# Optimization experiments

Hardware: AMD Instinct MI355X
Metric: run time of the kernel (lower is better)

Reference implementation:

```python
import jax, jax.numpy as jnp
import numpy as np

N_NODES = 50000
N_EDGES = 800000
IN_C, HID_C, OUT_C = 128, 128, 64


def setup_inputs() -> dict:
    key = jax.random.key(0)
    ks = jax.random.split(key, 12)
    glorot = lambda k, shape: jax.random.normal(k, shape, dtype=jnp.float32) * (2.0 / (shape[0] + shape[-1])) ** 0.5
    return {
        "x": jax.random.normal(ks[0], (N_NODES, IN_C), dtype=jnp.float32),
        "edge_index": jax.random.randint(ks[1], (2, N_EDGES), 0, N_NODES, dtype=jnp.int64),
        "W_s1": glorot(ks[2], (IN_C, HID_C)), "b_s1": jnp.zeros((HID_C,), jnp.float32),
        "W_s2": glorot(ks[3], (HID_C, HID_C)), "b_s2": jnp.zeros((HID_C,), jnp.float32),
        "W_m1": glorot(ks[4], (IN_C, HID_C)), "b_m1": jnp.zeros((HID_C,), jnp.float32),
        "W_m21": glorot(ks[5], (IN_C, HID_C)), "b_m21": jnp.zeros((HID_C,), jnp.float32),
        "W_m22": glorot(ks[6], (HID_C, HID_C)), "b_m22": jnp.zeros((HID_C,), jnp.float32),
        "W_att": glorot(ks[7], (HID_C, 1)), "b_att": jnp.zeros((1,), jnp.float32),
        "W_fc": glorot(ks[8], (2 * HID_C, OUT_C)), "b_fc": jnp.zeros((OUT_C,), jnp.float32),
    }


def _gcn_conv(x, W, b, src, dst, n_nodes):
    """PyG GCNConv: add self-loops, symmetric deg^-1/2 norm, linear, scatter-add, bias."""
    xw = x @ W  # [N, H]
    loop = jnp.arange(n_nodes, dtype=src.dtype)
    s = jnp.concatenate([src, loop])
    d = jnp.concatenate([dst, loop])
    ones = jnp.ones(s.shape[0], dtype=x.dtype)
    deg = jax.ops.segment_sum(ones, d, num_segments=n_nodes)  # in-degree incl. self loop
    dinv = jnp.where(deg > 0, jax.lax.rsqrt(deg), 0.0)
    norm = dinv[s] * dinv[d]  # [E+N]
    msg = xw[s] * norm[:, None]
    return jax.ops.segment_sum(msg, d, num_segments=n_nodes) + b


def reference(x, edge_index, W_s1, b_s1, W_s2, b_s2, W_m1, b_m1, W_m21, b_m21,
              W_m22, b_m22, W_att, b_att, W_fc, b_fc):
    n = x.shape[0]
    src, dst = edge_index[0], edge_index[1]
    # structural branch: two GCN layers
    h_struct = jax.nn.relu(_gcn_conv(x, W_s1, b_s1, src, dst, n))
    h_struct = jax.nn.relu(_gcn_conv(h_struct, W_s2, b_s2, src, dst, n))
    # meta branches
    h1 = jax.nn.relu(_gcn_conv(x, W_m1, b_m1, src, dst, n))
    h2 = jax.nn.relu(_gcn_conv(x, W_m21, b_m21, src, dst, n))
    h2 = jax.nn.relu(_gcn_conv(h2, W_m22, b_m22, src, dst, n))
    # attention-weighted fusion over the 2 branches
    H = jnp.stack([h1, h2], axis=1)  # [N, 2, H]
    attn_scores = H @ W_att + b_att  # [N, 2, 1]
    attn_weights = jax.nn.softmax(attn_scores, axis=1)
    h_meta = jnp.sum(attn_weights * H, axis=1)  # [N, H]
    h_comb = jnp.concatenate([h_struct, h_meta], axis=1)  # [N, 2H]
    return h_comb @ W_fc + b_fc  # [N, OUT_C]
```

## Files before the change

### kernel.cpp

```cpp
#include <hip/hip_runtime.h>
#include <hip/hip_bf16.h>

#define N_NODES 50000
#define N_EDGES 800000
#define IN_C 128
#define HID_C 128
#define OUT_C 64

#define SCAN_BS 256
#define SCAN_NB ((N_NODES + SCAN_BS - 1) / SCAN_BS)

typedef __attribute__((ext_vector_type(8))) short bf16x8;
typedef __attribute__((ext_vector_type(4))) float f32x4;

__device__ __forceinline__ ushort f2bf(float f) {
    unsigned u = __float_as_uint(f);
    return (ushort)((u + 0x7fffu + ((u >> 16) & 1u)) >> 16);
}
__device__ __forceinline__ float bf2f(ushort u) {
    return __uint_as_float(((unsigned)u) << 16);
}

__global__ void degree_kernel(const int* __restrict__ dst, int E, int* __restrict__ hist) {
    int e = blockIdx.x * blockDim.x + threadIdx.x;
    if (e < E) atomicAdd(&hist[dst[e]], 1);
}

__global__ void dinv_kernel(const int* __restrict__ hist, float* __restrict__ dinv, int n) {
    int i = blockIdx.x * blockDim.x + threadIdx.x;
    if (i < n) dinv[i] = rsqrtf((float)(hist[i] + 1));
}

__global__ __launch_bounds__(SCAN_BS)
void scan1_kernel(const int* __restrict__ hist, int* __restrict__ bsum, int n) {
    __shared__ int s[SCAN_BS];
    int t = threadIdx.x;
    int i = blockIdx.x * SCAN_BS + t;
    int v = (i < n) ? hist[i] : 0;
    s[t] = v;
    __syncthreads();
#pragma unroll
    for (int off = SCAN_BS / 2; off > 0; off >>= 1) {
        if (t < off) s[t] += s[t + off];
        __syncthreads();
    }
    if (t == 0) bsum[blockIdx.x] = s[0];
}

__global__ __launch_bounds__(SCAN_BS)
void scan2_kernel(int* __restrict__ bsum, int* __restrict__ bpre, int nb,
                  int* __restrict__ row_ptr_last, int n) {
    __shared__ int s[SCAN_BS];
    int t = threadIdx.x;
    int v = (t < nb) ? bsum[t] : 0;
    s[t] = v;
    __syncthreads();
#pragma unroll
    for (int off = 1; off < SCAN_BS; off <<= 1) {
        int tmp = (t >= off) ? s[t - off] : 0;
        __syncthreads();
        s[t] += tmp;
        __syncthreads();
    }
    if (t < nb) bpre[t] = s[t] - v;
    if (t == SCAN_BS - 1) row_ptr_last[n] = s[t];
}

__global__ __launch_bounds__(SCAN_BS)
void scan3_kernel(const int* __restrict__ hist, const int* __restrict__ bpre,
                  int* __restrict__ row_ptr, int* __restrict__ cursor, int n) {
    __shared__ int s[SCAN_BS];
    int t = threadIdx.x;
    int i = blockIdx.x * SCAN_BS + t;
    int v = (i < n) ? hist[i] : 0;
    s[t] = v;
    __syncthreads();
#pragma unroll
    for (int off = 1; off < SCAN_BS; off <<= 1) {
        int tmp = (t >= off) ? s[t - off] : 0;
        __syncthreads();
        s[t] += tmp;
        __syncthreads();
    }
    if (i < n) {
        int ex = s[t] - v + bpre[blockIdx.x];
        row_ptr[i] = ex;
        cursor[i]  = ex;
    }
}

__global__ void fill_kernel(const int* __restrict__ src, const int* __restrict__ dst, int E,
                            int* __restrict__ cursor, int2* __restrict__ edge_data,
                            const float* __restrict__ dinv) {
    int e = blockIdx.x * blockDim.x + threadIdx.x;
    if (e < E) {
        int d = dst[e];
        int s = src[e];
        int pos = atomicAdd(&cursor[d], 1);
        edge_data[pos] = make_int2(s, __float_as_int(dinv[s]));
    }
}

__global__ void cvt_bf16_kernel(const float* __restrict__ in, uint2* __restrict__ out, int n4) {
    int i = blockIdx.x * blockDim.x + threadIdx.x;
    if (i >= n4) return;
    float4 v = *(const float4*)&in[(size_t)i * 4];
    uint2 o;
    o.x = (uint)f2bf(v.x) | ((uint)f2bf(v.y) << 16);
    o.y = (uint)f2bf(v.z) | ((uint)f2bf(v.w) << 16);
    out[i] = o;
}

__global__ void pack_wcat_kernel(const float* __restrict__ Ws1, const float* __restrict__ Wm21,
                                 const float* __restrict__ Wm1,
                                 const float* __restrict__ bs1, const float* __restrict__ bm21,
                                 const float* __restrict__ bm1,
                                 ushort* __restrict__ Wt, float* __restrict__ bcat) {
    int idx = blockIdx.x * blockDim.x + threadIdx.x;
    if (idx < 384 * 128) {
        int c = idx >> 7, k = idx & 127;
        float v = (c < 128) ? Ws1[k * 128 + c]
                : (c < 256) ? Wm21[k * 128 + (c - 128)]
                            : Wm1[k * 128 + (c - 256)];
        Wt[idx] = f2bf(v);
    }
    if (idx < 384) {
        bcat[idx] = (idx < 128) ? bs1[idx] : (idx < 256) ? bm21[idx - 128] : bm1[idx - 256];
    }
}

__global__ void tpack_kernel(const float* __restrict__ W, ushort* __restrict__ Wt, int K, int C) {
    int idx = blockIdx.x * blockDim.x + threadIdx.x;
    if (idx >= K * C) return;
    int c = idx / K, k = idx % K;
    Wt[idx] = f2bf(W[(size_t)k * C + c]);
}

template<int C>
__global__ __launch_bounds__(256)
void agg_bf16(const ushort* __restrict__ X, int ldx,
              ushort* __restrict__ Y, int ldy,
              const int* __restrict__ row_ptr,
              const int2* __restrict__ edge_data,
              const float* __restrict__ dinv, int n) {
    constexpr int CG = C / 8;
    constexpr int SLOTS = 64 / CG;
    const int wid = blockIdx.x * (blockDim.x >> 6) + (threadIdx.x >> 6);
    if (wid >= n) return;
    const int lane = threadIdx.x & 63;
    const int cg = lane & (CG - 1);
    const int slot = lane / CG;

    const float di = dinv[wid];
    float acc[8] = {0.f, 0.f, 0.f, 0.f, 0.f, 0.f, 0.f, 0.f};

    auto fma_row = [&](uint4 v, float w) {
        acc[0] = fmaf(w, __uint_as_float(v.x << 16), acc[0]);
        acc[1] = fmaf(w, __uint_as_float(v.x & 0xffff0000u), acc[1]);
        acc[2] = fmaf(w, __uint_as_float(v.y << 16), acc[2]);
        acc[3] = fmaf(w, __uint_as_float(v.y & 0xffff0000u), acc[3]);
        acc[4] = fmaf(w, __uint_as_float(v.z << 16), acc[4]);
        acc[5] = fmaf(w, __uint_as_float(v.z & 0xffff0000u), acc[5]);
        acc[6] = fmaf(w, __uint_as_float(v.w << 16), acc[6]);
        acc[7] = fmaf(w, __uint_as_float(v.w & 0xffff0000u), acc[7]);
    };

    if (slot == 0) {
        uint4 v = *(const uint4*)&X[(size_t)wid * ldx + cg * 8];
        fma_row(v, di * di);
    }
    const int e0 = row_ptr[wid], e1 = row_ptr[wid + 1];
    int e = e0 + slot;
    for (; e + 3 * SLOTS < e1; e += 4 * SLOTS) {
        const int2 d0 = edge_data[e];
        const int2 d1 = edge_data[e + SLOTS];
        const int2 d2 = edge_data[e + 2 * SLOTS];
        const int2 d3 = edge_data[e + 3 * SLOTS];
        const uint4 v0 = *(const uint4*)&X[(size_t)d0.x * ldx + cg * 8];
        const uint4 v1 = *(const uint4*)&X[(size_t)d1.x * ldx + cg * 8];
        const uint4 v2 = *(const uint4*)&X[(size_t)d2.x * ldx + cg * 8];
        const uint4 v3 = *(const uint4*)&X[(size_t)d3.x * ldx + cg * 8];
        fma_row(v0, di * __int_as_float(d0.y));
        fma_row(v1, di * __int_as_float(d1.y));
        fma_row(v2, di * __int_as_float(d2.y));
        fma_row(v3, di * __int_as_float(d3.y));
    }
    for (; e < e1; e += SLOTS) {
        const int2 d0 = edge_data[e];
        const uint4 v0 = *(const uint4*)&X[(size_t)d0.x * ldx + cg * 8];
        fma_row(v0, di * __int_as_float(d0.y));
    }
#pragma unroll
    for (int j = 0; j < 8; ++j) {
        if (SLOTS == 4) acc[j] += __shfl_xor(acc[j], 16);
        if (SLOTS >= 2) acc[j] += __shfl_xor(acc[j], 32);
    }
    if (slot == 0) {
        uint4 o;
        o.x = (uint)f2bf(acc[0]) | ((uint)f2bf(acc[1]) << 16);
        o.y = (uint)f2bf(acc[2]) | ((uint)f2bf(acc[3]) << 16);
        o.z = (uint)f2bf(acc[4]) | ((uint)f2bf(acc[5]) << 16);
        o.w = (uint)f2bf(acc[6]) | ((uint)f2bf(acc[7]) << 16);
        *(uint4*)&Y[(size_t)wid * ldy + cg * 8] = o;
    }
}

__global__ __launch_bounds__(256)
void mfma_gemm_kernel(const ushort* __restrict__ A, int lda,
                      const ushort* __restrict__ Wt,
                      const float* __restrict__ bias,
                      void* __restrict__ Yv, int ldy,
                      int M, int relu, int obf16) {
    __shared__ char Asmem[128 * 272];
    const int tid = threadIdx.x;
    const int lane = tid & 63;
    const int w = tid >> 6;
    const int rb = blockIdx.x * 128;
    const int cb = blockIdx.y * 128;

    {
        const int rowbase = tid >> 4;
        const int inrow = (tid & 15) * 8;
#pragma unroll
        for (int it = 0; it < 8; ++it) {
            int row = it * 16 + rowbase;
            uint4 v = make_uint4(0u, 0u, 0u, 0u);
            int r = rb + row;
            if (r < M) v = *(const uint4*)&A[(size_t)r * lda + inrow];
            *(uint4*)&Asmem[row * 272 + (tid & 15) * 16] = v;
        }
    }
    __syncthreads();

    f32x4 acc[2][8];
#pragma unroll
    for (int i = 0; i < 2; ++i)
#pragma unroll
        for (int j = 0; j < 8; ++j) acc[i][j] = (f32x4){0.f, 0.f, 0.f, 0.f};

    const int arow0 = w * 32 + (lane & 15);
    const int kq = (lane >> 4) * 8;
    const int ccol = lane & 15;
#pragma unroll
    for (int ks = 0; ks < 4; ++ks) {
        const int k0 = ks * 32;
        const bf16x8 a0 = *(const bf16x8*)&Asmem[arow0 * 272 + (k0 + kq) * 2];
        const bf16x8 a1 = *(const bf16x8*)&Asmem[(arow0 + 16) * 272 + (k0 + kq) * 2];
#pragma unroll
        for (int ct = 0; ct < 8; ++ct) {
            const bf16x8 b = *(const bf16x8*)&Wt[(size_t)(cb + ct * 16 + ccol) * 128 + k0 + kq];
            acc[0][ct] = __builtin_amdgcn_mfma_f32_16x16x32_bf16(a0, b, acc[0][ct], 0, 0, 0);
            acc[1][ct] = __builtin_amdgcn_mfma_f32_16x16x32_bf16(a1, b, acc[1][ct], 0, 0, 0);
        }
    }

    const int rowq = (lane >> 4) * 4;
#pragma unroll
    for (int rt = 0; rt < 2; ++rt) {
#pragma unroll
        for (int ct = 0; ct < 8; ++ct) {
            const int col = cb + ct * 16 + ccol;
            const float bcol = bias[col];
#pragma unroll
            for (int r = 0; r < 4; ++r) {
                const int row = rb + w * 32 + rt * 16 + rowq + r;
                if (row >= M) continue;
                float v = acc[rt][ct][r] + bcol;
                if (relu) v = fmaxf(v, 0.f);
                if (obf16) ((ushort*)Yv)[(size_t)row * ldy + col] = f2bf(v);
                else       ((float*)Yv)[(size_t)row * ldy + col] = v;
            }
        }
    }
}

__global__ __launch_bounds__(256)
void mfma_fc_kernel(const ushort* __restrict__ A,
                    const ushort* __restrict__ Wt,
                    const float* __restrict__ bias,
                    float* __restrict__ Y, int M) {
    __shared__ char Asmem[64 * 528];
    const int tid = threadIdx.x;
    const int lane = tid & 63;
    const int w = tid >> 6;
    const int rb = blockIdx.x * 64;

    {
        const int rowbase = tid >> 5;
        const int seg = (tid & 31);
#pragma unroll
        for (int it = 0; it < 8; ++it) {
            int row = it * 8 + rowbase;
            uint4 v = make_uint4(0u, 0u, 0u, 0u);
            int r = rb + row;
            if (r < M) v = *(const uint4*)&A[(size_t)r * 256 + seg * 8];
            *(uint4*)&Asmem[row * 528 + seg * 16] = v;
        }
    }
    __syncthreads();

    f32x4 acc[4];
#pragma unroll
    for (int j = 0; j < 4; ++j) acc[j] = (f32x4){0.f, 0.f, 0.f, 0.f};

    const int arow = w * 16 + (lane & 15);
    const int kq = (lane >> 4) * 8;
    const int ccol = lane & 15;
#pragma unroll
    for (int ks = 0; ks < 8; ++ks) {
        const int k0 = ks * 32;
        const bf16x8 a = *(const bf16x8*)&Asmem[arow * 528 + (k0 + kq) * 2];
#pragma unroll
        for (int ct = 0; ct < 4; ++ct) {
            const bf16x8 b = *(const bf16x8*)&Wt[(size_t)(ct * 16 + ccol) * 256 + k0 + kq];
            acc[ct] = __builtin_amdgcn_mfma_f32_16x16x32_bf16(a, b, acc[ct], 0, 0, 0);
        }
    }

    const int rowq = (lane >> 4) * 4;
#pragma unroll
    for (int ct = 0; ct < 4; ++ct) {
        const int col = ct * 16 + ccol;
        const float bcol = bias[col];
#pragma unroll
        for (int r = 0; r < 4; ++r) {
            const int row = rb + w * 16 + rowq + r;
            if (row < M) Y[(size_t)row * 64 + col] = acc[ct][r] + bcol;
        }
    }
}

__global__ __launch_bounds__(64)
void attn_kernel(const ushort* __restrict__ h1bf, const ushort* __restrict__ h2bf,
                 const float* __restrict__ Watt, const float* __restrict__ batt,
                 ushort* __restrict__ outb, int ldout) {
    int i = blockIdx.x;
    int l = threadIdx.x;
    const ushort* h1p = &h1bf[(size_t)i * 384 + 256];
    const ushort* h2p = &h2bf[(size_t)i * 128];
    float w0 = Watt[l], w1w = Watt[l + 64];
    float h1a = bf2f(h1p[l]), h1b = bf2f(h1p[l + 64]);
    float h2a = bf2f(h2p[l]), h2b = bf2f(h2p[l + 64]);
    float a = h1a * w0 + h1b * w1w;
    float b = h2a * w0 + h2b * w1w;
#pragma unroll
    for (int off = 32; off > 0; off >>= 1) {
        a += __shfl_xor(a, off);
        b += __shfl_xor(b, off);
    }
    float ba = batt[0];
    a += ba; b += ba;
    float m  = fmaxf(a, b);
    float ea = __expf(a - m), eb = __expf(b - m);
    float inv = 1.f / (ea + eb);
    float wa = ea * inv, wb = eb * inv;
    outb[(size_t)i * ldout + l]      = f2bf(wa * h1a + wb * h2a);
    outb[(size_t)i * ldout + l + 64] = f2bf(wa * h1b + wb * h2b);
}

extern "C" void kernel_launch(void* const* d_in, const int* in_sizes, int n_in,
                              void* d_out, int out_size, void* d_ws, size_t ws_size,
                              hipStream_t stream) {
    const int N = N_NODES, E = N_EDGES;
    const float* x     = (const float*)d_in[0];
    const int*   ei    = (const int*)d_in[1];
    const int*   esrc  = ei;
    const int*   edst  = ei + E;
    const float* W_s1  = (const float*)d_in[2];
    const float* b_s1  = (const float*)d_in[3];
    const float* W_s2  = (const float*)d_in[4];
    const float* b_s2  = (const float*)d_in[5];
    const float* W_m1  = (const float*)d_in[6];
    const float* b_m1  = (const float*)d_in[7];
    const float* W_m21 = (const float*)d_in[8];
    const float* b_m21 = (const float*)d_in[9];
    const float* W_m22 = (const float*)d_in[10];
    const float* b_m22 = (const float*)d_in[11];
    const float* W_att = (const float*)d_in[12];
    const float* b_att = (const float*)d_in[13];
    const float* W_fc  = (const float*)d_in[14];
    const float* b_fc  = (const float*)d_in[15];
    float* out = (float*)d_out;

    char* base = (char*)d_ws;
    size_t off = 0;
    auto take = [&](size_t nbytes) -> void* {
        void* p = base + off;
        off += (nbytes + 255) & ~(size_t)255;
        return p;
    };
    int*    hist      = (int*)take((size_t)N * 4);
    int*    cursor    = (int*)take((size_t)N * 4);
    int*    row_ptr   = (int*)take((size_t)(N + 1) * 4);
    int*    bsum      = (int*)take((size_t)SCAN_NB * 4);
    int*    bpre      = (int*)take((size_t)SCAN_NB * 4);
    int2*   edge_data = (int2*)take((size_t)E * 8);
    float*  dinv      = (float*)take((size_t)N * 4);
    ushort* xb        = (ushort*)take((size_t)N * 128 * 2);
    ushort* agg_x     = (ushort*)take((size_t)N * 128 * 2);
    ushort* cat1      = (ushort*)take((size_t)N * 384 * 2);
    ushort* bufB      = (ushort*)take((size_t)N * 256 * 2);
    ushort* comb      = (ushort*)take((size_t)N * 256 * 2);
    ushort* h2buf     = (ushort*)take((size_t)N * 128 * 2);
    ushort* Wcat_t    = (ushort*)take((size_t)384 * 128 * 2);
    ushort* Ws2_t     = (ushort*)take((size_t)128 * 128 * 2);
    ushort* Wm22_t    = (ushort*)take((size_t)128 * 128 * 2);
    ushort* Wfc_t     = (ushort*)take((size_t)64 * 256 * 2);
    float*  bcat      = (float*)take((size_t)384 * 4);

    hipMemsetAsync(hist, 0, (size_t)N * 4, stream);
    degree_kernel<<<(E + 255) / 256, 256, 0, stream>>>(edst, E, hist);
    dinv_kernel<<<(N + 255) / 256, 256, 0, stream>>>(hist, dinv, N);
    scan1_kernel<<<SCAN_NB, SCAN_BS, 0, stream>>>(hist, bsum, N);
    scan2_kernel<<<1, SCAN_BS, 0, stream>>>(bsum, bpre, SCAN_NB, row_ptr, N);
    scan3_kernel<<<SCAN_NB, SCAN_BS, 0, stream>>>(hist, bpre, row_ptr, cursor, N);
    fill_kernel<<<(E + 255) / 256, 256, 0, stream>>>(esrc, edst, E, cursor, edge_data, dinv);

    cvt_bf16_kernel<<<(N * 128 / 4 + 255) / 256, 256, 0, stream>>>(x, (uint2*)xb, N * 128 / 4);
    pack_wcat_kernel<<<(384 * 128 + 255) / 256, 256, 0, stream>>>(W_s1, W_m21, W_m1,
                                                                  b_s1, b_m21, b_m1, Wcat_t, bcat);
    tpack_kernel<<<(128 * 128 + 255) / 256, 256, 0, stream>>>(W_s2, Ws2_t, 128, 128);
    tpack_kernel<<<(128 * 128 + 255) / 256, 256, 0, stream>>>(W_m22, Wm22_t, 128, 128);
    tpack_kernel<<<(256 * 64 + 255) / 256, 256, 0, stream>>>(W_fc, Wfc_t, 256, 64);

    agg_bf16<128><<<(N + 3) / 4, 256, 0, stream>>>(xb, 128, agg_x, 128, row_ptr, edge_data, dinv, N);

    dim3 gm384((N + 127) / 128, 3);
    dim3 gm128((N + 127) / 128, 1);
    mfma_gemm_kernel<<<gm384, 256, 0, stream>>>(agg_x, 128, Wcat_t, bcat, cat1, 384, N, 1, 1);

    agg_bf16<256><<<(N + 3) / 4, 256, 0, stream>>>(cat1, 384, bufB, 256, row_ptr, edge_data, dinv, N);

    mfma_gemm_kernel<<<gm128, 256, 0, stream>>>(bufB, 256, Ws2_t, b_s2, comb, 256, N, 1, 1);
    mfma_gemm_kernel<<<gm128, 256, 0, stream>>>(bufB + 128, 256, Wm22_t, b_m22, h2buf, 128, N, 1, 1);

    attn_kernel<<<N, 64, 0, stream>>>(cat1, h2buf, W_att, b_att, comb + 128, 256);

    mfma_fc_kernel<<<(N + 63) / 64, 256, 0, stream>>>(comb, Wfc_t, b_fc, out, N);
}
```

Measured before the change: 414.0 us.

## Fuse preprocessing kernels, collapse scan passes, and fuse second-layer GEMMs with attention

Merges x conversion, degree histogram and all weight packing into one multi-role prep kernel, and folds the dinv computation into scan1. The single-block scan2 is removed: each scan3 block now sums the preceding block totals itself. The two second-layer GEMMs and the attention fusion kernel become one gemm2 kernel whose second branch computes the attention softmax in its epilogue, so the h2 intermediate buffer is gone. This cuts launch count and one round-trip of h2 through memory, at the cost of redundant prefix summation in scan3 and an extra read of h1 in the GEMM epilogue.

```diff
diff --git a/kernel.cpp b/kernel.cpp
--- a/kernel.cpp
+++ b/kernel.cpp
@@ -10,6 +10,12 @@
 #define SCAN_BS 256
 #define SCAN_NB ((N_NODES + SCAN_BS - 1) / SCAN_BS)
 
+#define PREP_CVT_NB   6250
+#define PREP_DEG_NB   3125
+#define PREP_WCAT_NB  192
+#define PREP_TP_NB    64
+#define PREP_NB (PREP_CVT_NB + PREP_DEG_NB + PREP_WCAT_NB + 3 * PREP_TP_NB)
+
 typedef __attribute__((ext_vector_type(8))) short bf16x8;
 typedef __attribute__((ext_vector_type(4))) float f32x4;
 
@@ -21,22 +27,64 @@
     return __uint_as_float(((unsigned)u) << 16);
 }
 
-__global__ void degree_kernel(const int* __restrict__ dst, int E, int* __restrict__ hist) {
-    int e = blockIdx.x * blockDim.x + threadIdx.x;
-    if (e < E) atomicAdd(&hist[dst[e]], 1);
-}
-
-__global__ void dinv_kernel(const int* __restrict__ hist, float* __restrict__ dinv, int n) {
-    int i = blockIdx.x * blockDim.x + threadIdx.x;
-    if (i < n) dinv[i] = rsqrtf((float)(hist[i] + 1));
+__global__ __launch_bounds__(256)
+void prep_kernel(const float* __restrict__ x, uint2* __restrict__ xb4,
+                 const int* __restrict__ edst, int* __restrict__ hist,
+                 const float* __restrict__ Ws1, const float* __restrict__ Wm21,
+                 const float* __restrict__ Wm1,
+                 const float* __restrict__ bs1, const float* __restrict__ bm21,
+                 const float* __restrict__ bm1,
+                 ushort* __restrict__ Wcat_t, float* __restrict__ bcat,
+                 const float* __restrict__ Ws2, ushort* __restrict__ Ws2t,
+                 const float* __restrict__ Wm22, ushort* __restrict__ Wm22t,
+                 const float* __restrict__ Wfc, ushort* __restrict__ Wfct,
+                 int* __restrict__ row_ptr) {
+    const int bid = blockIdx.x;
+    const int t = threadIdx.x;
+    if (bid < PREP_CVT_NB) {
+        int i = bid * 256 + t;
+        float4 v = *(const float4*)&x[(size_t)i * 4];
+        uint2 o;
+        o.x = (uint)f2bf(v.x) | ((uint)f2bf(v.y) << 16);
+        o.y = (uint)f2bf(v.z) | ((uint)f2bf(v.w) << 16);
+        xb4[i] = o;
+    } else if (bid < PREP_CVT_NB + PREP_DEG_NB) {
+        int e = (bid - PREP_CVT_NB) * 256 + t;
+        atomicAdd(&hist[edst[e]], 1);
+    } else if (bid < PREP_CVT_NB + PREP_DEG_NB + PREP_WCAT_NB) {
+        int idx = (bid - PREP_CVT_NB - PREP_DEG_NB) * 256 + t;
+        int c = idx >> 7, k = idx & 127;
+        float v = (c < 128) ? Ws1[k * 128 + c]
+                : (c < 256) ? Wm21[k * 128 + (c - 128)]
+                            : Wm1[k * 128 + (c - 256)];
+        Wcat_t[idx] = f2bf(v);
+        if (idx < 384) {
+            bcat[idx] = (idx < 128) ? bs1[idx] : (idx < 256) ? bm21[idx - 128] : bm1[idx - 256];
+        }
+        if (idx == 0) row_ptr[N_NODES] = N_EDGES;
+    } else if (bid < PREP_CVT_NB + PREP_DEG_NB + PREP_WCAT_NB + PREP_TP_NB) {
+        int idx = (bid - PREP_CVT_NB - PREP_DEG_NB - PREP_WCAT_NB) * 256 + t;
+        int c = idx >> 7, k = idx & 127;
+        Ws2t[idx] = f2bf(Ws2[(size_t)k * 128 + c]);
+    } else if (bid < PREP_CVT_NB + PREP_DEG_NB + PREP_WCAT_NB + 2 * PREP_TP_NB) {
+        int idx = (bid - PREP_CVT_NB - PREP_DEG_NB - PREP_WCAT_NB - PREP_TP_NB) * 256 + t;
+        int c = idx >> 7, k = idx & 127;
+        Wm22t[idx] = f2bf(Wm22[(size_t)k * 128 + c]);
+    } else {
+        int idx = (bid - PREP_CVT_NB - PREP_DEG_NB - PREP_WCAT_NB - 2 * PREP_TP_NB) * 256 + t;
+        int c = idx >> 8, k = idx & 255;
+        Wfct[idx] = f2bf(Wfc[(size_t)k * 64 + c]);
+    }
 }
 
 __global__ __launch_bounds__(SCAN_BS)
-void scan1_kernel(const int* __restrict__ hist, int* __restrict__ bsum, int n) {
+void scan1_kernel(const int* __restrict__ hist, int* __restrict__ bsum,
+                  float* __restrict__ dinv, int n) {
     __shared__ int s[SCAN_BS];
     int t = threadIdx.x;
     int i = blockIdx.x * SCAN_BS + t;
     int v = (i < n) ? hist[i] : 0;
+    if (i < n) dinv[i] = rsqrtf((float)(v + 1));
     s[t] = v;
     __syncthreads();
 #pragma unroll
@@ -48,11 +96,27 @@
 }
 
 __global__ __launch_bounds__(SCAN_BS)
-void scan2_kernel(int* __restrict__ bsum, int* __restrict__ bpre, int nb,
-                  int* __restrict__ row_ptr_last, int n) {
+void scan3_kernel(const int* __restrict__ hist, const int* __restrict__ bsum,
+                  int* __restrict__ row_ptr, int* __restrict__ cursor, int n) {
     __shared__ int s[SCAN_BS];
+    __shared__ int pre_s;
     int t = threadIdx.x;
-    int v = (t < nb) ? bsum[t] : 0;
+    int b = blockIdx.x;
+    int p = 0;
+    for (int j = t; j < b; j += SCAN_BS) p += bsum[j];
+    s[t] = p;
+    __syncthreads();
+#pragma unroll
+    for (int off = SCAN_BS / 2; off > 0; off >>= 1) {
+        if (t < off) s[t] += s[t + off];
+        __syncthreads();
+    }
+    if (t == 0) pre_s = s[0];
+    __syncthreads();
+    const int pre = pre_s;
+    __syncthreads();
+    int i = b * SCAN_BS + t;
+    int v = (i < n) ? hist[i] : 0;
     s[t] = v;
     __syncthreads();
 #pragma unroll
@@ -62,28 +126,8 @@
         s[t] += tmp;
         __syncthreads();
     }
-    if (t < nb) bpre[t] = s[t] - v;
-    if (t == SCAN_BS - 1) row_ptr_last[n] = s[t];
-}
-
-__global__ __launch_bounds__(SCAN_BS)
-void scan3_kernel(const int* __restrict__ hist, const int* __restrict__ bpre,
-                  int* __restrict__ row_ptr, int* __restrict__ cursor, int n) {
-    __shared__ int s[SCAN_BS];
-    int t = threadIdx.x;
-    int i = blockIdx.x * SCAN_BS + t;
-    int v = (i < n) ? hist[i] : 0;
-    s[t] = v;
-    __syncthreads();
-#pragma unroll
-    for (int off = 1; off < SCAN_BS; off <<= 1) {
-        int tmp = (t >= off) ? s[t - off] : 0;
-        __syncthreads();
-        s[t] += tmp;
-        __syncthreads();
-    }
     if (i < n) {
-        int ex = s[t] - v + bpre[blockIdx.x];
+        int ex = s[t] - v + pre;
         row_ptr[i] = ex;
         cursor[i]  = ex;
     }
@@ -99,41 +143,6 @@
         int pos = atomicAdd(&cursor[d], 1);
         edge_data[pos] = make_int2(s, __float_as_int(dinv[s]));
     }
-}
-
-__global__ void cvt_bf16_kernel(const float* __restrict__ in, uint2* __restrict__ out, int n4) {
-    int i = blockIdx.x * blockDim.x + threadIdx.x;
-    if (i >= n4) return;
-    float4 v = *(const float4*)&in[(size_t)i * 4];
-    uint2 o;
-    o.x = (uint)f2bf(v.x) | ((uint)f2bf(v.y) << 16);
-    o.y = (uint)f2bf(v.z) | ((uint)f2bf(v.w) << 16);
-    out[i] = o;
-}
-
-__global__ void pack_wcat_kernel(const float* __restrict__ Ws1, const float* __restrict__ Wm21,
-                                 const float* __restrict__ Wm1,
-                                 const float* __restrict__ bs1, const float* __restrict__ bm21,
-                                 const float* __restrict__ bm1,
-                                 ushort* __restrict__ Wt, float* __restrict__ bcat) {
-    int idx = blockIdx.x * blockDim.x + threadIdx.x;
-    if (idx < 384 * 128) {
-        int c = idx >> 7, k = idx & 127;
-        float v = (c < 128) ? Ws1[k * 128 + c]
-                : (c < 256) ? Wm21[k * 128 + (c - 128)]
-                            : Wm1[k * 128 + (c - 256)];
-        Wt[idx] = f2bf(v);
-    }
-    if (idx < 384) {
-        bcat[idx] = (idx < 128) ? bs1[idx] : (idx < 256) ? bm21[idx - 128] : bm1[idx - 256];
-    }
-}
-
-__global__ void tpack_kernel(const float* __restrict__ W, ushort* __restrict__ Wt, int K, int C) {
-    int idx = blockIdx.x * blockDim.x + threadIdx.x;
-    if (idx >= K * C) return;
-    int c = idx / K, k = idx % K;
-    Wt[idx] = f2bf(W[(size_t)k * C + c]);
 }
 
 template<int C>
@@ -275,6 +284,125 @@
 }
 
 __global__ __launch_bounds__(256)
+void gemm2_kernel(const ushort* __restrict__ bufB,
+                  const ushort* __restrict__ Ws2t, const float* __restrict__ bs2,
+                  const ushort* __restrict__ Wm22t, const float* __restrict__ bm22,
+                  const ushort* __restrict__ cat1,
+                  const float* __restrict__ Watt, const float* __restrict__ batt,
+                  ushort* __restrict__ comb, int M) {
+    __shared__ char Asmem[128 * 272];
+    const int tid = threadIdx.x;
+    const int lane = tid & 63;
+    const int w = tid >> 6;
+    const int rb = blockIdx.x * 128;
+    const int branch = blockIdx.y;
+    const ushort* A = bufB + (branch ? 128 : 0);
+    const ushort* Wt = branch ? Wm22t : Ws2t;
+    const float* bias = branch ? bm22 : bs2;
+
+    {
+        const int rowbase = tid >> 4;
+        const int seg = tid & 15;
+#pragma unroll
+        for (int it = 0; it < 8; ++it) {
+            int row = it * 16 + rowbase;
+            uint4 v = make_uint4(0u, 0u, 0u, 0u);
+            int r = rb + row;
+            if (r < M) v = *(const uint4*)&A[(size_t)r * 256 + seg * 8];
+            *(uint4*)&Asmem[row * 272 + seg * 16] = v;
+        }
+    }
+    __syncthreads();
+
+    f32x4 acc[2][8];
+#pragma unroll
+    for (int i = 0; i < 2; ++i)
+#pragma unroll
+        for (int j = 0; j < 8; ++j) acc[i][j] = (f32x4){0.f, 0.f, 0.f, 0.f};
+
+    const int arow0 = w * 32 + (lane & 15);
+    const int kq = (lane >> 4) * 8;
+    const int ccol = lane & 15;
+#pragma unroll
+    for (int ks = 0; ks < 4; ++ks) {
+        const int k0 = ks * 32;
+        const bf16x8 a0 = *(const bf16x8*)&Asmem[arow0 * 272 + (k0 + kq) * 2];
+        const bf16x8 a1 = *(const bf16x8*)&Asmem[(arow0 + 16) * 272 + (k0 + kq) * 2];
+#pragma unroll
+        for (int ct = 0; ct < 8; ++ct) {
+            const bf16x8 b = *(const bf16x8*)&Wt[(size_t)(ct * 16 + ccol) * 128 + k0 + kq];
+            acc[0][ct] = __builtin_amdgcn_mfma_f32_16x16x32_bf16(a0, b, acc[0][ct], 0, 0, 0);
+            acc[1][ct] = __builtin_amdgcn_mfma_f32_16x16x32_bf16(a1, b, acc[1][ct], 0, 0, 0);
+        }
+    }
+
+    const int quad = lane >> 4;
+    if (branch == 0) {
+#pragma unroll
+        for (int rt = 0; rt < 2; ++rt) {
+#pragma unroll
+            for (int ct = 0; ct < 8; ++ct) {
+                const int col = ct * 16 + ccol;
+                const float bcol = bias[col];
+#pragma unroll
+                for (int r = 0; r < 4; ++r) {
+                    const int row = rb + w * 32 + rt * 16 + quad * 4 + r;
+                    if (row >= M) continue;
+                    comb[(size_t)row * 256 + col] = f2bf(fmaxf(acc[rt][ct][r] + bcol, 0.f));
+                }
+            }
+        }
+    } else {
+#pragma unroll
+        for (int rt = 0; rt < 2; ++rt)
+#pragma unroll
+            for (int ct = 0; ct < 8; ++ct) {
+                const float bcol = bias[ct * 16 + ccol];
+#pragma unroll
+                for (int r = 0; r < 4; ++r)
+                    acc[rt][ct][r] = fmaxf(acc[rt][ct][r] + bcol, 0.f);
+            }
+        float wv[8];
+#pragma unroll
+        for (int ct = 0; ct < 8; ++ct) wv[ct] = Watt[ct * 16 + ccol];
+        const float ba = batt[0];
+#pragma unroll
+        for (int rt = 0; rt < 2; ++rt) {
+#pragma unroll
+            for (int r = 0; r < 4; ++r) {
+                const int row0 = rb + w * 32 + rt * 16 + quad * 4 + r;
+                const int rowc = (row0 < M) ? row0 : (M - 1);
+                const ushort* h1row = &cat1[(size_t)rowc * 384 + 256];
+                float bp = 0.f, ap = 0.f;
+#pragma unroll
+                for (int ct = 0; ct < 8; ++ct) {
+                    bp += acc[rt][ct][r] * wv[ct];
+                    ap += bf2f(h1row[ct * 16 + ccol]) * wv[ct];
+                }
+#pragma unroll
+                for (int off = 1; off < 16; off <<= 1) {
+                    bp += __shfl_xor(bp, off);
+                    ap += __shfl_xor(ap, off);
+                }
+                const float a = ap + ba, b = bp + ba;
+                const float m = fmaxf(a, b);
+                const float ea = __expf(a - m), eb = __expf(b - m);
+                const float inv = 1.f / (ea + eb);
+                const float wa = ea * inv, wb = eb * inv;
+                if (row0 < M) {
+#pragma unroll
+                    for (int ct = 0; ct < 8; ++ct) {
+                        const float h1 = bf2f(h1row[ct * 16 + ccol]);
+                        comb[(size_t)row0 * 256 + 128 + ct * 16 + ccol] =
+                            f2bf(fmaf(wa, h1, wb * acc[rt][ct][r]));
+                    }
+                }
+            }
+        }
+    }
+}
+
+__global__ __launch_bounds__(256)
 void mfma_fc_kernel(const ushort* __restrict__ A,
                     const ushort* __restrict__ Wt,
                     const float* __restrict__ bias,
@@ -328,34 +456,6 @@
             if (row < M) Y[(size_t)row * 64 + col] = acc[ct][r] + bcol;
         }
     }
-}
-
-__global__ __launch_bounds__(64)
-void attn_kernel(const ushort* __restrict__ h1bf, const ushort* __restrict__ h2bf,
-                 const float* __restrict__ Watt, const float* __restrict__ batt,
-                 ushort* __restrict__ outb, int ldout) {
-    int i = blockIdx.x;
-    int l = threadIdx.x;
-    const ushort* h1p = &h1bf[(size_t)i * 384 + 256];
-    const ushort* h2p = &h2bf[(size_t)i * 128];
-    float w0 = Watt[l], w1w = Watt[l + 64];
-    float h1a = bf2f(h1p[l]), h1b = bf2f(h1p[l + 64]);
-    float h2a = bf2f(h2p[l]), h2b = bf2f(h2p[l + 64]);
-    float a = h1a * w0 + h1b * w1w;
-    float b = h2a * w0 + h2b * w1w;
-#pragma unroll
-    for (int off = 32; off > 0; off >>= 1) {
-        a += __shfl_xor(a, off);
-        b += __shfl_xor(b, off);
-    }
-    float ba = batt[0];
-    a += ba; b += ba;
-    float m  = fmaxf(a, b);
-    float ea = __expf(a - m), eb = __expf(b - m);
-    float inv = 1.f / (ea + eb);
-    float wa = ea * inv, wb = eb * inv;
-    outb[(size_t)i * ldout + l]      = f2bf(wa * h1a + wb * h2a);
-    outb[(size_t)i * ldout + l + 64] = f2bf(wa * h1b + wb * h2b);
 }
 
 extern "C" void kernel_launch(void* const* d_in, const int* in_sizes, int n_in,
@@ -393,7 +493,6 @@
     int*    cursor    = (int*)take((size_t)N * 4);
     int*    row_ptr   = (int*)take((size_t)(N + 1) * 4);
     int*    bsum      = (int*)take((size_t)SCAN_NB * 4);
-    int*    bpre      = (int*)take((size_t)SCAN_NB * 4);
     int2*   edge_data = (int2*)take((size_t)E * 8);
     float*  dinv      = (float*)take((size_t)N * 4);
     ushort* xb        = (ushort*)take((size_t)N * 128 * 2);
@@ -401,7 +500,6 @@
     ushort* cat1      = (ushort*)take((size_t)N * 384 * 2);
     ushort* bufB      = (ushort*)take((size_t)N * 256 * 2);
     ushort* comb      = (ushort*)take((size_t)N * 256 * 2);
-    ushort* h2buf     = (ushort*)take((size_t)N * 128 * 2);
     ushort* Wcat_t    = (ushort*)take((size_t)384 * 128 * 2);
     ushort* Ws2_t     = (ushort*)take((size_t)128 * 128 * 2);
     ushort* Wm22_t    = (ushort*)take((size_t)128 * 128 * 2);
@@ -409,32 +507,20 @@
     float*  bcat      = (float*)take((size_t)384 * 4);
 
     hipMemsetAsync(hist, 0, (size_t)N * 4, stream);
-    degree_kernel<<<(E + 255) / 256, 256, 0, stream>>>(edst, E, hist);
-    dinv_kernel<<<(N + 255) / 256, 256, 0, stream>>>(hist, dinv, N);
-    scan1_kernel<<<SCAN_NB, SCAN_BS, 0, stream>>>(hist, bsum, N);
-    scan2_kernel<<<1, SCAN_BS, 0, stream>>>(bsum, bpre, SCAN_NB, row_ptr, N);
-    scan3_kernel<<<SCAN_NB, SCAN_BS, 0, stream>>>(hist, bpre, row_ptr, cursor, N);
+    prep_kernel<<<PREP_NB, 256, 0, stream>>>(x, (uint2*)xb, edst, hist,
+                                             W_s1, W_m21, W_m1, b_s1, b_m21, b_m1,
+                                             Wcat_t, bcat, W_s2, Ws2_t, W_m22, Wm22_t,
+                                             W_fc, Wfc_t, row_ptr);
+    scan1_kernel<<<SCAN_NB, SCAN_BS, 0, stream>>>(hist, bsum, dinv, N);
+    scan3_kernel<<<SCAN_NB, SCAN_BS, 0, stream>>>(hist, bsum, row_ptr, cursor, N);
     fill_kernel<<<(E + 255) / 256, 256, 0, stream>>>(esrc, edst, E, cursor, edge_data, dinv);
 
-    cvt_bf16_kernel<<<(N * 128 / 4 + 255) / 256, 256, 0, stream>>>(x, (uint2*)xb, N * 128 / 4);
-    pack_wcat_kernel<<<(384 * 128 + 255) / 256, 256, 0, stream>>>(W_s1, W_m21, W_m1,
-                                                                  b_s1, b_m21, b_m1, Wcat_t, bcat);
-    tpack_kernel<<<(128 * 128 + 255) / 256, 256, 0, stream>>>(W_s2, Ws2_t, 128, 128);
-    tpack_kernel<<<(128 * 128 + 255) / 256, 256, 0, stream>>>(W_m22, Wm22_t, 128, 128);
-    tpack_kernel<<<(256 * 64 + 255) / 256, 256, 0, stream>>>(W_fc, Wfc_t, 256, 64);
-
     agg_bf16<128><<<(N + 3) / 4, 256, 0, stream>>>(xb, 128, agg_x, 128, row_ptr, edge_data, dinv, N);
-
     dim3 gm384((N + 127) / 128, 3);
-    dim3 gm128((N + 127) / 128, 1);
     mfma_gemm_kernel<<<gm384, 256, 0, stream>>>(agg_x, 128, Wcat_t, bcat, cat1, 384, N, 1, 1);
-
     agg_bf16<256><<<(N + 3) / 4, 256, 0, stream>>>(cat1, 384, bufB, 256, row_ptr, edge_data, dinv, N);
-
-    mfma_gemm_kernel<<<gm128, 256, 0, stream>>>(bufB, 256, Ws2_t, b_s2, comb, 256, N, 1, 1);
-    mfma_gemm_kernel<<<gm128, 256, 0, stream>>>(bufB + 128, 256, Wm22_t, b_m22, h2buf, 128, N, 1, 1);
-
-    attn_kernel<<<N, 64, 0, stream>>>(cat1, h2buf, W_att, b_att, comb + 128, 256);
-
+    dim3 gm2((N + 127) / 128, 2);
+    gemm2_kernel<<<gm2, 256, 0, stream>>>(bufB, Ws2_t, b_s2, Wm22_t, b_m22,
+                                          cat1, W_att, b_att, comb, N);
     mfma_fc_kernel<<<(N + 63) / 64, 256, 0, stream>>>(comb, Wfc_t, b_fc, out, N);
 }
```

Result: faster. 383.6 us (-7.4%).
